# Optimization experiments

Measured on AMD Instinct MI355X. Metric: run time of the kernel, lower is better.

## Reference

```python
import jax, jax.numpy as jnp
import numpy as np

NUM_MODULES = 4
EXPERTS_PER_MODULE = 4
TOTAL_EXPERTS = NUM_MODULES * EXPERTS_PER_MODULE
TOP_K = 4
NORM_TOPK_PROB = True
T = 32768
D = 1536


def setup_inputs() -> dict:
    key = jax.random.key(0)
    k1, k2, k3 = jax.random.split(key, 3)
    hidden_states = jax.random.normal(k1, (T, D), dtype=jnp.float32)
    # nn.Linear weights: (out_features, in_features)
    Wm = jax.random.normal(k2, (NUM_MODULES, D), dtype=jnp.float32) * 0.02
    We = jax.random.normal(k3, (TOTAL_EXPERTS, D), dtype=jnp.float32) * 0.02
    return {"hidden_states": hidden_states, "Wm": Wm, "We": We}


def reference(hidden_states, Wm, We):
    Tn = hidden_states.shape[0]
    # Stage 1: module routing
    module_logits = jnp.einsum('td,md->tm', hidden_states, Wm)  # (T, num_modules)
    module_probs = jax.nn.softmax(module_logits.astype(jnp.float32), axis=-1)
    # Stage 2: expert routing, grouped per module (intra-module softmax)
    expert_logits = jnp.einsum('td,ed->te', hidden_states, We)  # (T, total_experts)
    expert_logits = expert_logits.reshape(Tn, NUM_MODULES, EXPERTS_PER_MODULE)
    expert_probs = jax.nn.softmax(expert_logits.astype(jnp.float32), axis=-1)
    # Combined hierarchical distribution
    combined_probs = (module_probs[:, :, None] * expert_probs).reshape(Tn, TOTAL_EXPERTS)
    # Top-k over flat combined distribution
    top_k_weights, top_k_indices = jax.lax.top_k(combined_probs, TOP_K)
    if NORM_TOPK_PROB:
        top_k_weights = top_k_weights / (jnp.sum(top_k_weights, axis=-1, keepdims=True) + 1e-8)
    top_k_weights = top_k_weights.astype(hidden_states.dtype)
    return combined_probs, top_k_weights, top_k_indices
```

## Files before the change

### kernel.cpp

```cpp
#include <hip/hip_runtime.h>
#include <math.h>


#define DD 1536
#define NM 4
#define NE 16
#define NW 20
#define NTHR 256
#define RPB 32
#define NJ 24
#define SJ 4
#define NSTAGE 6
#define WL_F (SJ * NW * 64)

typedef float v4f __attribute__((ext_vector_type(4)));

__device__ __forceinline__ void wstage(float* wl, const float* We, const float* Wm,
                                       int tid, int s)
{
#pragma unroll
    for (int it = 0; it < 5; it++) {
        const int off = tid * 4 + it * 1024;
        const int jw  = off / 1280;
        const int rem = off - jw * 1280;
        const int e   = rem >> 6;
        const int qc  = rem & 63;
        const int col = (s * SJ + jw) * 64 + qc;
        v4f w = (e < NE) ? *(const v4f*)(We + (size_t)e * DD + col)
                         : *(const v4f*)(Wm + (size_t)(e - NE) * DD + col);
        *(v4f*)&wl[off] = w;
    }
}

__device__ __forceinline__ void jstep(const float* wl, int jw, int q,
                                      v4f ha, v4f hb, float* accA, float* accB)
{
    const float* wb = &wl[jw * 1280 + q * 4];
#pragma unroll
    for (int eg = 0; eg < 5; eg++) {
        v4f w0 = *(const v4f*)(wb + (eg * 4 + 0) * 64);
        v4f w1 = *(const v4f*)(wb + (eg * 4 + 1) * 64);
        v4f w2 = *(const v4f*)(wb + (eg * 4 + 2) * 64);
        v4f w3 = *(const v4f*)(wb + (eg * 4 + 3) * 64);
        float* aA = accA + eg * 4;
        float* aB = accB + eg * 4;
        aA[0] = fmaf(ha.x, w0.x, aA[0]); aA[0] = fmaf(ha.y, w0.y, aA[0]);
        aA[0] = fmaf(ha.z, w0.z, aA[0]); aA[0] = fmaf(ha.w, w0.w, aA[0]);
        aA[1] = fmaf(ha.x, w1.x, aA[1]); aA[1] = fmaf(ha.y, w1.y, aA[1]);
        aA[1] = fmaf(ha.z, w1.z, aA[1]); aA[1] = fmaf(ha.w, w1.w, aA[1]);
        aA[2] = fmaf(ha.x, w2.x, aA[2]); aA[2] = fmaf(ha.y, w2.y, aA[2]);
        aA[2] = fmaf(ha.z, w2.z, aA[2]); aA[2] = fmaf(ha.w, w2.w, aA[2]);
        aA[3] = fmaf(ha.x, w3.x, aA[3]); aA[3] = fmaf(ha.y, w3.y, aA[3]);
        aA[3] = fmaf(ha.w, w3.w, aA[3]); aA[3] = fmaf(ha.z, w3.z, aA[3]);
        aB[0] = fmaf(hb.x, w0.x, aB[0]); aB[0] = fmaf(hb.y, w0.y, aB[0]);
        aB[0] = fmaf(hb.z, w0.z, aB[0]); aB[0] = fmaf(hb.w, w0.w, aB[0]);
        aB[1] = fmaf(hb.x, w1.x, aB[1]); aB[1] = fmaf(hb.y, w1.y, aB[1]);
        aB[1] = fmaf(hb.z, w1.z, aB[1]); aB[1] = fmaf(hb.w, w1.w, aB[1]);
        aB[2] = fmaf(hb.x, w2.x, aB[2]); aB[2] = fmaf(hb.y, w2.y, aB[2]);
        aB[2] = fmaf(hb.z, w2.z, aB[2]); aB[2] = fmaf(hb.w, w2.w, aB[2]);
        aB[3] = fmaf(hb.x, w3.x, aB[3]); aB[3] = fmaf(hb.y, w3.y, aB[3]);
        aB[3] = fmaf(hb.z, w3.z, aB[3]); aB[3] = fmaf(hb.w, w3.w, aB[3]);
    }
}

__global__ __launch_bounds__(NTHR)
void router_kernel(const float* __restrict__ hs,
                   const float* __restrict__ Wm,
                   const float* __restrict__ We,
                   float* __restrict__ out,
                   int T)
{
    __shared__ __align__(16) float wl[WL_F];
    const int tid  = threadIdx.x;
    const int wv   = tid >> 6;
    const int lane = tid & 63;
    const int q    = lane & 15;
    const int g    = lane >> 4;
    const int rW   = blockIdx.x * RPB + wv * 8;

    const float* hsA = hs + (size_t)(rW + g) * DD + q * 4;
    const float* hsB = hsA + (size_t)4 * DD;

    float accA[NW], accB[NW];
#pragma unroll
    for (int e = 0; e < NW; e++) { accA[e] = 0.f; accB[e] = 0.f; }

    v4f a0 = *(const v4f*)(hsA);
    v4f b0 = *(const v4f*)(hsB);
    v4f a1 = *(const v4f*)(hsA + 64);
    v4f b1 = *(const v4f*)(hsB + 64);

#pragma unroll 1
    for (int s = 0; s < NSTAGE; s++) {
        if (s) __syncthreads();
        wstage(wl, We, Wm, tid, s);
        __syncthreads();

        const int j0 = s * SJ;
        v4f a2 = *(const v4f*)(hsA + (size_t)(j0 + 2) * 64);
        v4f b2 = *(const v4f*)(hsB + (size_t)(j0 + 2) * 64);
        v4f a3 = *(const v4f*)(hsA + (size_t)(j0 + 3) * 64);
        v4f b3 = *(const v4f*)(hsB + (size_t)(j0 + 3) * 64);
        jstep(wl, 0, q, a0, b0, accA, accB);
        jstep(wl, 1, q, a1, b1, accA, accB);
        if (s + 1 < NSTAGE) {
            a0 = *(const v4f*)(hsA + (size_t)(j0 + 4) * 64);
            b0 = *(const v4f*)(hsB + (size_t)(j0 + 4) * 64);
            a1 = *(const v4f*)(hsA + (size_t)(j0 + 5) * 64);
            b1 = *(const v4f*)(hsB + (size_t)(j0 + 5) * 64);
        }
        jstep(wl, 2, q, a2, b2, accA, accB);
        jstep(wl, 3, q, a3, b3, accA, accB);
    }

#pragma unroll
    for (int e = 0; e < NW; e++) {
        accA[e] += __shfl_xor(accA[e], 1); accA[e] += __shfl_xor(accA[e], 2);
        accA[e] += __shfl_xor(accA[e], 4); accA[e] += __shfl_xor(accA[e], 8);
        accB[e] += __shfl_xor(accB[e], 1); accB[e] += __shfl_xor(accB[e], 2);
        accB[e] += __shfl_xor(accB[e], 4); accB[e] += __shfl_xor(accB[e], 8);
    }

    if (q < 2) {
        float logit[NW];
#pragma unroll
        for (int e = 0; e < NW; e++) logit[e] = q ? accB[e] : accA[e];
        const int row = rW + g + (q ? 4 : 0);

        float mmax = logit[16];
#pragma unroll
        for (int m = 1; m < NM; m++) mmax = fmaxf(mmax, logit[16 + m]);
        float mexp[NM], msum = 0.f;
#pragma unroll
        for (int m = 0; m < NM; m++) { mexp[m] = expf(logit[16 + m] - mmax); msum += mexp[m]; }

        float comb[NE];
#pragma unroll
        for (int m = 0; m < NM; m++) {
            float mprob = mexp[m] / msum;
            float emax = logit[m * 4];
#pragma unroll
            for (int jj = 1; jj < 4; jj++) emax = fmaxf(emax, logit[m * 4 + jj]);
            float ee[4], esum = 0.f;
#pragma unroll
            for (int jj = 0; jj < 4; jj++) { ee[jj] = expf(logit[m * 4 + jj] - emax); esum += ee[jj]; }
            float scale = mprob / esum;
#pragma unroll
            for (int jj = 0; jj < 4; jj++) comb[m * 4 + jj] = ee[jj] * scale;
        }

        float4* cw = (float4*)(out + (size_t)row * 16);
        cw[0] = make_float4(comb[0],  comb[1],  comb[2],  comb[3]);
        cw[1] = make_float4(comb[4],  comb[5],  comb[6],  comb[7]);
        cw[2] = make_float4(comb[8],  comb[9],  comb[10], comb[11]);
        cw[3] = make_float4(comb[12], comb[13], comb[14], comb[15]);

        float tv[4]; int ti[4];
        unsigned mask = 0;
#pragma unroll
        for (int k = 0; k < 4; k++) {
            float best = -1.f; int bi = 0;
#pragma unroll
            for (int i = 0; i < NE; i++) {
                bool avail = !((mask >> i) & 1u);
                if (avail && comb[i] > best) { best = comb[i]; bi = i; }
            }
            tv[k] = best; ti[k] = bi; mask |= 1u << bi;
        }
        float s = tv[0] + tv[1] + tv[2] + tv[3] + 1e-8f;

        const size_t wOff = (size_t)T * 16;
        const size_t iOff = (size_t)T * 20;
        float4* ww = (float4*)(out + wOff + (size_t)row * 4);
        *ww = make_float4(tv[0] / s, tv[1] / s, tv[2] / s, tv[3] / s);
        float4* iw = (float4*)(out + iOff + (size_t)row * 4);
        *iw = make_float4((float)ti[0], (float)ti[1], (float)ti[2], (float)ti[3]);
    }
}

extern "C" void kernel_launch(void* const* d_in, const int* in_sizes, int n_in,
                              void* d_out, int out_size, void* d_ws, size_t ws_size,
                              hipStream_t stream)
{
    const float* hs = (const float*)d_in[0];
    const float* Wm = (const float*)d_in[1];
    const float* We = (const float*)d_in[2];
    float* out = (float*)d_out;
    const int T = in_sizes[0] / DD;
    router_kernel<<<T / RPB, NTHR, 0, stream>>>(hs, Wm, We, out, T);
}
```

Measured before the change: 306.7 us.

## Double block size and stage weights in two large chunks with rolling prefetch

Result: faster. 294.1 us (-4.1%).

```diff
diff --git a/kernel.cpp b/kernel.cpp
--- a/kernel.cpp
+++ b/kernel.cpp
@@ -6,11 +6,12 @@
 #define NM 4
 #define NE 16
 #define NW 20
-#define NTHR 256
-#define RPB 32
+#define NTHR 512
+#define NWAVE 8
+#define RPB 64
 #define NJ 24
-#define SJ 4
-#define NSTAGE 6
+#define SJ 12
+#define NSTAGE 2
 #define WL_F (SJ * NW * 64)
 
 typedef float v4f __attribute__((ext_vector_type(4)));
@@ -19,16 +20,18 @@
                                        int tid, int s)
 {
 #pragma unroll
-    for (int it = 0; it < 5; it++) {
-        const int off = tid * 4 + it * 1024;
-        const int jw  = off / 1280;
-        const int rem = off - jw * 1280;
-        const int e   = rem >> 6;
-        const int qc  = rem & 63;
-        const int col = (s * SJ + jw) * 64 + qc;
-        v4f w = (e < NE) ? *(const v4f*)(We + (size_t)e * DD + col)
-                         : *(const v4f*)(Wm + (size_t)(e - NE) * DD + col);
-        *(v4f*)&wl[off] = w;
+    for (int it = 0; it < 8; it++) {
+        const int off = tid * 4 + it * 2048;
+        if (off < WL_F) {
+            const int jw  = off / 1280;
+            const int rem = off - jw * 1280;
+            const int e   = rem >> 6;
+            const int qc  = rem & 63;
+            const int col = (s * SJ + jw) * 64 + qc;
+            v4f w = (e < NE) ? *(const v4f*)(We + (size_t)e * DD + col)
+                             : *(const v4f*)(Wm + (size_t)(e - NE) * DD + col);
+            *(v4f*)&wl[off] = w;
+        }
     }
 }
 
@@ -51,7 +54,7 @@
         aA[2] = fmaf(ha.x, w2.x, aA[2]); aA[2] = fmaf(ha.y, w2.y, aA[2]);
         aA[2] = fmaf(ha.z, w2.z, aA[2]); aA[2] = fmaf(ha.w, w2.w, aA[2]);
         aA[3] = fmaf(ha.x, w3.x, aA[3]); aA[3] = fmaf(ha.y, w3.y, aA[3]);
-        aA[3] = fmaf(ha.w, w3.w, aA[3]); aA[3] = fmaf(ha.z, w3.z, aA[3]);
+        aA[3] = fmaf(ha.z, w3.z, aA[3]); aA[3] = fmaf(ha.w, w3.w, aA[3]);
         aB[0] = fmaf(hb.x, w0.x, aB[0]); aB[0] = fmaf(hb.y, w0.y, aB[0]);
         aB[0] = fmaf(hb.z, w0.z, aB[0]); aB[0] = fmaf(hb.w, w0.w, aB[0]);
         aB[1] = fmaf(hb.x, w1.x, aB[1]); aB[1] = fmaf(hb.y, w1.y, aB[1]);
@@ -90,27 +93,27 @@
     v4f a1 = *(const v4f*)(hsA + 64);
     v4f b1 = *(const v4f*)(hsB + 64);
 
+    wstage(wl, We, Wm, tid, 0);
+    __syncthreads();
+
 #pragma unroll 1
     for (int s = 0; s < NSTAGE; s++) {
-        if (s) __syncthreads();
-        wstage(wl, We, Wm, tid, s);
-        __syncthreads();
-
-        const int j0 = s * SJ;
-        v4f a2 = *(const v4f*)(hsA + (size_t)(j0 + 2) * 64);
-        v4f b2 = *(const v4f*)(hsB + (size_t)(j0 + 2) * 64);
-        v4f a3 = *(const v4f*)(hsA + (size_t)(j0 + 3) * 64);
-        v4f b3 = *(const v4f*)(hsB + (size_t)(j0 + 3) * 64);
-        jstep(wl, 0, q, a0, b0, accA, accB);
-        jstep(wl, 1, q, a1, b1, accA, accB);
-        if (s + 1 < NSTAGE) {
-            a0 = *(const v4f*)(hsA + (size_t)(j0 + 4) * 64);
-            b0 = *(const v4f*)(hsB + (size_t)(j0 + 4) * 64);
-            a1 = *(const v4f*)(hsA + (size_t)(j0 + 5) * 64);
-            b1 = *(const v4f*)(hsB + (size_t)(j0 + 5) * 64);
+        if (s) {
+            __syncthreads();
+            wstage(wl, We, Wm, tid, s);
+            __syncthreads();
         }
-        jstep(wl, 2, q, a2, b2, accA, accB);
-        jstep(wl, 3, q, a3, b3, accA, accB);
+#pragma unroll 1
+        for (int jj = 0; jj < SJ; jj++) {
+            const int j = s * SJ + jj;
+            v4f a2, b2;
+            if (j + 2 < NJ) {
+                a2 = *(const v4f*)(hsA + (size_t)(j + 2) * 64);
+                b2 = *(const v4f*)(hsB + (size_t)(j + 2) * 64);
+            }
+            jstep(wl, jj, q, a0, b0, accA, accB);
+            a0 = a1; b0 = b1; a1 = a2; b1 = b2;
+        }
     }
 
 #pragma unroll
```
